# Optimization experiments

Hardware: AMD Instinct MI355X
Metric: run time of the kernel (lower is better)

## Reference

```python
import jax, jax.numpy as jnp
import numpy as np

# Module hyperparameters derived from init_kwargs
G = 100          # grid_size = int(n_samples ** gamma) = int(10000 ** 0.5)
K = 3            # KAN_SPLINE_ORDER
NB = G + K       # num_basis = 103
H = (1.5 - (-0.5)) / G
# grid identical for every input feature (torch expands a 1D grid)
GRID = jnp.arange(-K, G + K + 1, dtype=jnp.float32) * H - 0.5  # (G + 2K + 1,)


def bspline_basis(x):
    """Cox-de Boor recursion. x: (B, F) -> (B, F, NB)."""
    g = GRID
    xe = x[..., None]  # (B, F, 1)
    bases = ((xe >= g[:-1]) & (xe < g[1:])).astype(x.dtype)  # (B, F, G+2K)
    for k in range(1, K + 1):
        left = (xe - g[:-(k + 1)]) / jnp.maximum(g[k:-1] - g[:-(k + 1)], 1e-8)
        right = (g[k + 1:] - xe) / jnp.maximum(g[k + 1:] - g[1:-k], 1e-8)
        bases = left * bases[..., :-1] + right * bases[..., 1:]
    return bases  # (B, F, NB)


def kan_layer(x, bw, sw, wb, ws, residual):
    # base path: SiLU activation then linear
    base_out = jax.nn.silu(x) @ bw.T                      # (B, out)
    # spline path: basis expansion then contraction with spline_weight
    spline_out = jnp.einsum('bin,oin->bo', bspline_basis(x), sw)
    out = wb * base_out + ws * spline_out
    return out + x if residual else out


def setup_inputs() -> dict:
    key = jax.random.key(0)
    ks = jax.random.split(key, 16)
    B, D, W = 2048, 64, 243
    inp = {'x': jax.random.uniform(ks[0], (B, D), dtype=jnp.float32)}
    dims = [(D, W), (W, W), (W, W), (W, W), (W, W), (W, 1)]
    for i, (fi, fo) in enumerate(dims):
        kb, ksw = jax.random.split(jax.random.fold_in(key, i + 1))
        inp[f'bw{i}'] = jax.random.normal(kb, (fo, fi), dtype=jnp.float32) * (1.0 / np.sqrt(fi))
        # torch init: uniform(-0.5/G, 0.5/G)
        inp[f'sw{i}'] = jax.random.uniform(ksw, (fo, fi, NB), dtype=jnp.float32,
                                           minval=-0.5 / G, maxval=0.5 / G)
        inp[f'wb{i}'] = jnp.zeros((1,), dtype=jnp.float32)
        inp[f'ws{i}'] = jnp.ones((1,), dtype=jnp.float32)
    return inp


def reference(x, bw0, sw0, wb0, ws0, bw1, sw1, wb1, ws1, bw2, sw2, wb2, ws2,
              bw3, sw3, wb3, ws3, bw4, sw4, wb4, ws4, bw5, sw5, wb5, ws5):
    layers = [
        (bw0, sw0, wb0, ws0, False),  # 64 -> 243 (in != out: no residual)
        (bw1, sw1, wb1, ws1, True),
        (bw2, sw2, wb2, ws2, True),
        (bw3, sw3, wb3, ws3, True),
        (bw4, sw4, wb4, ws4, True),
        (bw5, sw5, wb5, ws5, False),  # 243 -> 1 (use_residual=False)
    ]
    h = x
    for bw, sw, wb, ws, res in layers:
        h = kan_layer(h, bw, sw, wb, ws, res)
    return h
```

## Files before the change

kernel.cpp:

```cpp
#include <hip/hip_runtime.h>
#include <hip/hip_fp16.h>
#include <math.h>

#define BATCH 2048
#define NBAS 103
#define NPAIR 102
#define OUTR 243
#define OUTP 256

typedef _Float16 half2v __attribute__((ext_vector_type(2)));

__device__ __forceinline__ float dot2(unsigned a, unsigned b, float c) {
#if __has_builtin(__builtin_amdgcn_fdot2)
    return __builtin_amdgcn_fdot2(__builtin_bit_cast(half2v, a),
                                  __builtin_bit_cast(half2v, b), c, false);
#else
    __half2 ha = __builtin_bit_cast(__half2, a), hb = __builtin_bit_cast(__half2, b);
    c = fmaf(__low2float(ha), __low2float(hb), c);
    c = fmaf(__high2float(ha), __high2float(hb), c);
    return c;
#endif
}

__device__ __forceinline__ uint4 make_meta(float x, int i) {
    float u = (x + 0.56f) * 50.0f;
    bool inr = (u >= 0.0f) && (u < 106.0f);
    float fj = floorf(u);
    float t = u - fj;
    int j = (int)fj;
    j = j < -1 ? -1 : (j > 106 ? 106 : j);
    float omt = 1.0f - t;
    float t2 = t * t, t3 = t2 * t;
    float w[4];
    w[0] = omt * omt * omt * (1.0f / 6.0f);
    w[1] = (3.0f * t3 - 6.0f * t2 + 4.0f) * (1.0f / 6.0f);
    w[2] = (-3.0f * t3 + 3.0f * t2 + 3.0f * t + 1.0f) * (1.0f / 6.0f);
    w[3] = t3 * (1.0f / 6.0f);
    int idx = j - 3;
    int idxc = idx < 0 ? 0 : (idx > 99 ? 99 : idx);
    int d = idx - idxc;
    float wc[4];
    #pragma unroll
    for (int m = 0; m < 4; ++m) {
        int s = m - d;
        wc[m] = (inr && s >= 0 && s < 4) ? w[s] : 0.0f;
    }
    __half2 w01 = __floats2half2_rn(wc[0], wc[1]);
    __half2 w23 = __floats2half2_rn(wc[2], wc[3]);
    uint4 m4;
    m4.x = __builtin_bit_cast(unsigned, w01);
    m4.y = __builtin_bit_cast(unsigned, w23);
    m4.z = (unsigned)((i * NPAIR + idxc) << 8);
    m4.w = (unsigned)(i * NBAS + idxc);
    return m4;
}

__device__ __forceinline__ void pairgen_body(
    const float* __restrict__ sw, int IN, unsigned* __restrict__ pairT,
    __half (*tile)[106], int i, int obase)
{
    int nl = threadIdx.x & 63;
    int w = threadIdx.x >> 6;
    #pragma unroll
    for (int k = 0; k < 8; ++k) {
        int r = w * 8 + k;
        int o = obase + r;
        if (o < OUTR) {
            const float* p = sw + ((size_t)o * IN + i) * NBAS;
            tile[r][nl] = __float2half(p[nl]);
            if (nl + 64 < NBAS)
                tile[r][nl + 64] = __float2half(p[nl + 64]);
        }
    }
    __syncthreads();
    unsigned* dst = pairT + (size_t)i * NPAIR * 256 + obase;
    for (int idx = threadIdx.x; idx < NPAIR * 32; idx += 256) {
        int p = idx >> 5, o = idx & 31;
        unsigned v = 0;
        if (obase + o < OUTR) {
            unsigned lo = __half_as_ushort(tile[o][p]);
            unsigned hi = __half_as_ushort(tile[o][p + 1]);
            v = lo | (hi << 16);
        }
        dst[(size_t)p * 256 + o] = v;
    }
}

__global__ __launch_bounds__(256) void pairgen_kernel(
    const float* __restrict__ sw, int IN, unsigned* __restrict__ pairT)
{
    __shared__ __half tile[32][106];
    pairgen_body(sw, IN, pairT, tile, blockIdx.x, blockIdx.y * 32);
}

template <int IN>
__global__ __launch_bounds__(256) void basis_kernel(
    const float* __restrict__ xin, int xstride, uint4* __restrict__ meta,
    float4* __restrict__ zbuf)
{
    int e = blockIdx.x * 256 + threadIdx.x;
    if (zbuf && e < (BATCH * OUTP) / 4) zbuf[e] = make_float4(0.f, 0.f, 0.f, 0.f);
    if (e >= BATCH * IN) return;
    int b = e / IN, i = e - b * IN;
    meta[e] = make_meta(xin[(size_t)b * xstride + i], i);
}

template <bool ADDRES>
__global__ __launch_bounds__(256) void basis_mid_kernel(
    const float* __restrict__ hprev,
    const float* __restrict__ parts,
    uint4* __restrict__ meta, float* __restrict__ hcomb)
{
    int e = blockIdx.x * 256 + threadIdx.x;
    if (e >= BATCH * OUTR) return;
    int b = e / OUTR, i = e - b * OUTR;
    size_t addr = (size_t)b * OUTP + i;
    const size_t PS = (size_t)BATCH * OUTP;
    float h = ADDRES ? hprev[addr] : 0.0f;
    #pragma unroll
    for (int s = 0; s < 8; ++s) h += parts[s * PS + addr];
    hcomb[addr] = h;
    meta[e] = make_meta(h, i);
}

template <bool ADDRES>
__global__ __launch_bounds__(256) void fused_pg_bm_kernel(
    const float* __restrict__ sw, unsigned* __restrict__ pairT,
    const float* __restrict__ hprev, const float* __restrict__ parts,
    uint4* __restrict__ meta, float* __restrict__ hcomb)
{
    if (blockIdx.y == 0) {
        __shared__ __half tile[32][106];
        pairgen_body(sw, OUTR, pairT, tile, blockIdx.x >> 3, (blockIdx.x & 7) * 32);
    } else {
        int e = blockIdx.x * 256 + threadIdx.x;
        if (e >= BATCH * OUTR) return;
        int b = e / OUTR, i = e - b * OUTR;
        size_t addr = (size_t)b * OUTP + i;
        const size_t PS = (size_t)BATCH * OUTP;
        float h = ADDRES ? hprev[addr] : 0.0f;
        #pragma unroll
        for (int s = 0; s < 8; ++s) h += parts[s * PS + addr];
        hcomb[addr] = h;
        meta[e] = make_meta(h, i);
    }
}

__global__ __launch_bounds__(256) void fused0_kernel(
    const float* __restrict__ sw0, unsigned* __restrict__ pairT,
    const float* __restrict__ xin, uint4* __restrict__ meta)
{
    if (blockIdx.y == 0) {
        __shared__ __half tile[32][106];
        pairgen_body(sw0, 64, pairT, tile, blockIdx.x >> 3, (blockIdx.x & 7) * 32);
    } else {
        int e = blockIdx.x * 256 + threadIdx.x;
        int b = e >> 6, i = e & 63;
        meta[e] = make_meta(xin[(size_t)b * 64 + i], i);
    }
}

template <int IN>
__global__ __launch_bounds__(256, 8) void layer_store_kernel(
    const unsigned* __restrict__ pairT, const uint4* __restrict__ meta,
    const float* __restrict__ h_in, int hstride,
    const float* __restrict__ bw,
    const float* __restrict__ wbp, const float* __restrict__ wsp,
    float* __restrict__ part)
{
    const int lane = threadIdx.x & 63;
    const int wave = __builtin_amdgcn_readfirstlane(threadIdx.x >> 6);
    const int b0 = blockIdx.y * 8 + wave * 2;
    const int cx = blockIdx.x;
    const int i0 = (IN * cx) >> 3;
    const int i1 = (IN * (cx + 1)) >> 3;
    const uint4* mp0 = meta + (size_t)b0 * IN;
    const uint4* mp1 = mp0 + IN;
    float a0[4] = {0.f, 0.f, 0.f, 0.f};
    float a1[4] = {0.f, 0.f, 0.f, 0.f};
    #pragma unroll 2
    for (int i = i0; i < i1; ++i) {
        uint4 m0 = mp0[i];
        uint4 m1 = mp1[i];
        const uint4* pA = (const uint4*)(pairT + m0.z) + lane;
        const uint4* pB = (const uint4*)(pairT + m1.z) + lane;
        uint4 ra = pA[0];
        uint4 rb = pA[128];
        uint4 rc = pB[0];
        uint4 rd = pB[128];
        a0[0] = dot2(m0.x, ra.x, a0[0]); a0[1] = dot2(m0.x, ra.y, a0[1]);
        a0[2] = dot2(m0.x, ra.z, a0[2]); a0[3] = dot2(m0.x, ra.w, a0[3]);
        a0[0] = dot2(m0.y, rb.x, a0[0]); a0[1] = dot2(m0.y, rb.y, a0[1]);
        a0[2] = dot2(m0.y, rb.z, a0[2]); a0[3] = dot2(m0.y, rb.w, a0[3]);
        a1[0] = dot2(m1.x, rc.x, a1[0]); a1[1] = dot2(m1.x, rc.y, a1[1]);
        a1[2] = dot2(m1.x, rc.z, a1[2]); a1[3] = dot2(m1.x, rc.w, a1[3]);
        a1[0] = dot2(m1.y, rd.x, a1[0]); a1[1] = dot2(m1.y, rd.y, a1[1]);
        a1[2] = dot2(m1.y, rd.z, a1[2]); a1[3] = dot2(m1.y, rd.w, a1[3]);
    }
    float wsv = wsp[0];
    float wbv = wbp[0];
    float4 v0 = make_float4(wsv * a0[0], wsv * a0[1], wsv * a0[2], wsv * a0[3]);
    float4 v1 = make_float4(wsv * a1[0], wsv * a1[1], wsv * a1[2], wsv * a1[3]);
    if (wbv != 0.0f) {
        float* pv0 = &v0.x; float* pv1 = &v1.x;
        for (int c = 0; c < 4; ++c) {
            int o = lane * 4 + c;
            if (o < OUTR) {
                float bs0 = 0.0f, bs1 = 0.0f;
                for (int i = i0; i < i1; ++i) {
                    float x0 = h_in[(size_t)b0 * hstride + i];
                    float x1 = h_in[(size_t)(b0 + 1) * hstride + i];
                    bs0 = fmaf(x0 / (1.0f + expf(-x0)), bw[o * IN + i], bs0);
                    bs1 = fmaf(x1 / (1.0f + expf(-x1)), bw[o * IN + i], bs1);
                }
                pv0[c] += wbv * bs0;
                pv1[c] += wbv * bs1;
            }
        }
    }
    float* d0 = part + ((size_t)cx * BATCH + b0) * OUTP + lane * 4;
    *(float4*)d0 = v0;
    *(float4*)(d0 + OUTP) = v1;
}

template <int IN, bool RES>
__global__ __launch_bounds__(256, 8) void layer_atomic_kernel(
    const unsigned* __restrict__ pairT, const uint4* __restrict__ meta,
    const float* __restrict__ h_in, int hstride,
    const float* __restrict__ bw,
    const float* __restrict__ wbp, const float* __restrict__ wsp,
    float* __restrict__ out)
{
    const int lane = threadIdx.x & 63;
    const int wave = __builtin_amdgcn_readfirstlane(threadIdx.x >> 6);
    const int b = blockIdx.y * 4 + wave;
    const int cx = blockIdx.x;
    const int i0 = (IN * cx) >> 3;
    const int i1 = (IN * (cx + 1)) >> 3;
    const uint4* mp = meta + (size_t)b * IN;
    float acc[4] = {0.f, 0.f, 0.f, 0.f};
    #pragma unroll 2
    for (int i = i0; i < i1; ++i) {
        uint4 m = mp[i];
        const uint4* pA = (const uint4*)(pairT + m.z) + lane;
        uint4 ra = pA[0];
        uint4 rb = pA[128];
        acc[0] = dot2(m.x, ra.x, acc[0]); acc[1] = dot2(m.x, ra.y, acc[1]);
        acc[2] = dot2(m.x, ra.z, acc[2]); acc[3] = dot2(m.x, ra.w, acc[3]);
        acc[0] = dot2(m.y, rb.x, acc[0]); acc[1] = dot2(m.y, rb.y, acc[1]);
        acc[2] = dot2(m.y, rb.z, acc[2]); acc[3] = dot2(m.y, rb.w, acc[3]);
    }
    float wsv = wsp[0];
    float wbv = wbp[0];
    #pragma unroll
    for (int c = 0; c < 4; ++c) {
        int o = lane * 4 + c;
        float v = wsv * acc[c];
        if (RES && cx == 0) v += h_in[(size_t)b * hstride + o];
        if (wbv != 0.0f && o < OUTR) {
            float bs = 0.0f;
            for (int i = i0; i < i1; ++i) {
                float xx = h_in[(size_t)b * hstride + i];
                bs = fmaf(xx / (1.0f + expf(-xx)), bw[o * IN + i], bs);
            }
            v += wbv * bs;
        }
        unsafeAtomicAdd(&out[(size_t)b * OUTP + o], v);
    }
}

__global__ __launch_bounds__(256) void final_kernel(
    const float* __restrict__ sw5,
    const uint4* __restrict__ meta,
    const float* __restrict__ h, const float* __restrict__ bw5,
    const float* __restrict__ wbp, const float* __restrict__ wsp,
    float* __restrict__ out)
{
    int wave = threadIdx.x >> 6, lane = threadIdx.x & 63;
    int b = blockIdx.x * 4 + wave;
    float s = 0.0f;
    for (int i = lane; i < OUTR; i += 64) {
        uint4 m = meta[(size_t)b * OUTR + i];
        __half2 w01 = __builtin_bit_cast(__half2, m.x);
        __half2 w23 = __builtin_bit_cast(__half2, m.y);
        const float* p = sw5 + m.w;
        s += __low2float(w01) * p[0] + __high2float(w01) * p[1]
           + __low2float(w23) * p[2] + __high2float(w23) * p[3];
    }
    #pragma unroll
    for (int d = 32; d; d >>= 1) s += __shfl_down(s, d, 64);
    if (lane == 0) {
        float v = wsp[0] * s;
        float wbv = wbp[0];
        if (wbv != 0.0f) {
            float bs = 0.0f;
            for (int i = 0; i < OUTR; ++i) {
                float xx = h[(size_t)b * OUTP + i];
                bs = fmaf(xx / (1.0f + expf(-xx)), bw5[i], bs);
            }
            v += wbv * bs;
        }
        out[b] = v;
    }
}

extern "C" void kernel_launch(void* const* d_in, const int* in_sizes, int n_in,
                              void* d_out, int out_size, void* d_ws, size_t ws_size,
                              hipStream_t stream)
{
    const float* x = (const float*)d_in[0];
    const float *bw[6], *sw[6], *wb[6], *ws[6];
    for (int l = 0; l < 6; ++l) {
        bw[l] = (const float*)d_in[1 + 4 * l];
        sw[l] = (const float*)d_in[2 + 4 * l];
        wb[l] = (const float*)d_in[3 + 4 * l];
        ws[l] = (const float*)d_in[4 + 4 * l];
    }
    char* base = (char*)d_ws;
    const size_t PAIR_B = 0;
    const size_t META_B = 25380864;
    unsigned* pairT = (unsigned*)(base + PAIR_B);
    uint4*    meta  = (uint4*)(base + META_B);
    float*    outp  = (float*)d_out;

    const size_t NEED_NEW = 54315008;
    const int NB243 = (BATCH * OUTR + 255) / 256;

    if (ws_size >= NEED_NEW) {
        float* parts = (float*)(base + 33343488);
        float* hcA   = (float*)(base + 50120704);
        float* hcB   = (float*)(base + 52217856);

        fused0_kernel<<<dim3(512, 2), 256, 0, stream>>>(sw[0], pairT, x, meta);
        layer_store_kernel<64><<<dim3(8, BATCH / 8), 256, 0, stream>>>(
            pairT, meta, x, 64, bw[0], wb[0], ws[0], parts);

        float* hin = hcA; float* hout = hcB;
        for (int l = 1; l <= 4; ++l) {
            if (l == 1)
                fused_pg_bm_kernel<false><<<dim3(1944, 2), 256, 0, stream>>>(
                    sw[l], pairT, nullptr, parts, meta, hin);
            else
                fused_pg_bm_kernel<true><<<dim3(1944, 2), 256, 0, stream>>>(
                    sw[l], pairT, hout, parts, meta, hin);
            layer_store_kernel<243><<<dim3(8, BATCH / 8), 256, 0, stream>>>(
                pairT, meta, hin, OUTP, bw[l], wb[l], ws[l], parts);
            float* tmp = hin; hin = hout; hout = tmp;
        }
        basis_mid_kernel<true><<<NB243, 256, 0, stream>>>(hout, parts, meta, hin);
        final_kernel<<<BATCH / 4, 256, 0, stream>>>(sw[5], meta, hin, bw[5], wb[5], ws[5], outp);
    } else {
        if (ws_size < (size_t)37537792) return;
        float* hA = (float*)(base + 33343488);
        float* hB = (float*)(base + 35440640);
        pairgen_kernel<<<dim3(64, 8), 256, 0, stream>>>(sw[0], 64, pairT);
        basis_kernel<64><<<(BATCH * 64) / 256, 256, 0, stream>>>(x, 64, meta, (float4*)hA);
        layer_atomic_kernel<64, false><<<dim3(8, BATCH / 4), 256, 0, stream>>>(
            pairT, meta, x, 64, bw[0], wb[0], ws[0], hA);
        float* hin = hA; float* hout = hB;
        for (int l = 1; l <= 4; ++l) {
            pairgen_kernel<<<dim3(OUTR, 8), 256, 0, stream>>>(sw[l], OUTR, pairT);
            basis_kernel<243><<<NB243, 256, 0, stream>>>(hin, OUTP, meta, (float4*)hout);
            layer_atomic_kernel<243, true><<<dim3(8, BATCH / 4), 256, 0, stream>>>(
                pairT, meta, hin, OUTP, bw[l], wb[l], ws[l], hout);
            float* tmp = hin; hin = hout; hout = tmp;
        }
        basis_kernel<243><<<NB243, 256, 0, stream>>>(hin, OUTP, meta, nullptr);
        final_kernel<<<BATCH / 4, 256, 0, stream>>>(sw[5], meta, hin, bw[5], wb[5], ws[5], outp);
    }
}
```

Baseline: 400.0 us.

## Precompute all layer spline pair tables in one launch and fuse final basis

When the workspace is large enough, a single kernel converts the spline weights of layers 0 to 4 into fp16 pair tables, each in its own buffer, and also builds the layer-0 basis metadata. The per-layer fused pairgen-plus-basis launches become plain basis_mid launches. Separately, the last basis pass and final kernel merge into one kernel that sums the partials, evaluates the basis inline and does the reduction. This removes kernel launches and the serial dependency of each layer's weight conversion on the previous layer, at the cost of about 83 MB more workspace and a large up-front conversion launch. If the harness workspace is smaller, the old path runs with only the final fusion.

```diff
diff --git a/kernel.cpp b/kernel.cpp
--- a/kernel.cpp
+++ b/kernel.cpp
@@ -91,6 +91,36 @@
 {
     __shared__ __half tile[32][106];
     pairgen_body(sw, IN, pairT, tile, blockIdx.x, blockIdx.y * 32);
+}
+
+__global__ __launch_bounds__(256) void pairgen_all_kernel(
+    const float* __restrict__ sw0, const float* __restrict__ sw1,
+    const float* __restrict__ sw2, const float* __restrict__ sw3,
+    const float* __restrict__ sw4,
+    unsigned* __restrict__ pT0, unsigned* __restrict__ pT1,
+    unsigned* __restrict__ pT2, unsigned* __restrict__ pT3,
+    unsigned* __restrict__ pT4,
+    const float* __restrict__ xin, uint4* __restrict__ meta)
+{
+    __shared__ __half tile[32][106];
+    int bx = blockIdx.x;
+    if (bx < 512) {
+        pairgen_body(sw0, 64, pT0, tile, bx >> 3, (bx & 7) * 32);
+    } else if (bx < 8288) {
+        int idx = bx - 512;
+        int l = idx / 1944;
+        int rem = idx - l * 1944;
+        const float* sw; unsigned* pt;
+        if (l == 0)      { sw = sw1; pt = pT1; }
+        else if (l == 1) { sw = sw2; pt = pT2; }
+        else if (l == 2) { sw = sw3; pt = pT3; }
+        else             { sw = sw4; pt = pT4; }
+        pairgen_body(sw, OUTR, pt, tile, rem >> 3, (rem & 7) * 32);
+    } else {
+        int e = (bx - 8288) * 256 + threadIdx.x;
+        int b = e >> 6, i = e & 63;
+        meta[e] = make_meta(xin[(size_t)b * 64 + i], i);
+    }
 }
 
 template <int IN>
@@ -269,6 +299,39 @@
     }
 }
 
+__global__ __launch_bounds__(256) void final_fused_kernel(
+    const float* __restrict__ sw5,
+    const float* __restrict__ hprev,
+    const float* __restrict__ parts,
+    const float* __restrict__ bw5,
+    const float* __restrict__ wbp, const float* __restrict__ wsp,
+    float* __restrict__ out)
+{
+    int wave = threadIdx.x >> 6, lane = threadIdx.x & 63;
+    int b = blockIdx.x * 4 + wave;
+    const size_t PS = (size_t)BATCH * OUTP;
+    float s = 0.0f, bs = 0.0f;
+    for (int i = lane; i < OUTR; i += 64) {
+        size_t addr = (size_t)b * OUTP + i;
+        float h = hprev[addr];
+        #pragma unroll
+        for (int ss = 0; ss < 8; ++ss) h += parts[ss * PS + addr];
+        uint4 m = make_meta(h, i);
+        __half2 w01 = __builtin_bit_cast(__half2, m.x);
+        __half2 w23 = __builtin_bit_cast(__half2, m.y);
+        const float* p = sw5 + m.w;
+        s += __low2float(w01) * p[0] + __high2float(w01) * p[1]
+           + __low2float(w23) * p[2] + __high2float(w23) * p[3];
+        bs = fmaf(h / (1.0f + expf(-h)), bw5[i], bs);
+    }
+    #pragma unroll
+    for (int d = 32; d; d >>= 1) {
+        s += __shfl_down(s, d, 64);
+        bs += __shfl_down(bs, d, 64);
+    }
+    if (lane == 0) out[b] = wsp[0] * s + wbp[0] * bs;
+}
+
 __global__ __launch_bounds__(256) void final_kernel(
     const float* __restrict__ sw5,
     const uint4* __restrict__ meta,
@@ -317,52 +380,81 @@
         ws[l] = (const float*)d_in[4 + 4 * l];
     }
     char* base = (char*)d_ws;
-    const size_t PAIR_B = 0;
-    const size_t META_B = 25380864;
-    unsigned* pairT = (unsigned*)(base + PAIR_B);
-    uint4*    meta  = (uint4*)(base + META_B);
-    float*    outp  = (float*)d_out;
-
-    const size_t NEED_NEW = 54315008;
+    unsigned* pairT1 = (unsigned*)(base + 0);
+    uint4*    meta   = (uint4*)(base + 25380864);
+    float*    outp   = (float*)d_out;
     const int NB243 = (BATCH * OUTR + 255) / 256;
 
-    if (ws_size >= NEED_NEW) {
+    const size_t NEED_ALL = 137142272;
+    const size_t NEED_MID = 54315008;
+    const size_t NEED_ATM = 37537792;
+
+    if (ws_size >= NEED_ALL) {
+        float*    parts  = (float*)(base + 33343488);
+        float*    hcA    = (float*)(base + 50120704);
+        float*    hcB    = (float*)(base + 52217856);
+        unsigned* pairT0 = (unsigned*)(base + 54315008);
+        unsigned* pairT2 = (unsigned*)(base + 60999680);
+        unsigned* pairT3 = (unsigned*)(base + 86380544);
+        unsigned* pairT4 = (unsigned*)(base + 111761408);
+        unsigned* pT[5] = {pairT0, pairT1, pairT2, pairT3, pairT4};
+
+        pairgen_all_kernel<<<8800, 256, 0, stream>>>(
+            sw[0], sw[1], sw[2], sw[3], sw[4],
+            pairT0, pairT1, pairT2, pairT3, pairT4, x, meta);
+
+        layer_store_kernel<64><<<dim3(8, BATCH / 8), 256, 0, stream>>>(
+            pairT0, meta, x, 64, bw[0], wb[0], ws[0], parts);
+
+        float* hin = hcA; float* hout = hcB;
+        for (int l = 1; l <= 4; ++l) {
+            if (l == 1)
+                basis_mid_kernel<false><<<NB243, 256, 0, stream>>>(nullptr, parts, meta, hin);
+            else
+                basis_mid_kernel<true><<<NB243, 256, 0, stream>>>(hout, parts, meta, hin);
+            layer_store_kernel<243><<<dim3(8, BATCH / 8), 256, 0, stream>>>(
+                pT[l], meta, hin, OUTP, bw[l], wb[l], ws[l], parts);
+            float* tmp = hin; hin = hout; hout = tmp;
+        }
+        final_fused_kernel<<<BATCH / 4, 256, 0, stream>>>(
+            sw[5], hout, parts, bw[5], wb[5], ws[5], outp);
+    } else if (ws_size >= NEED_MID) {
         float* parts = (float*)(base + 33343488);
         float* hcA   = (float*)(base + 50120704);
         float* hcB   = (float*)(base + 52217856);
 
-        fused0_kernel<<<dim3(512, 2), 256, 0, stream>>>(sw[0], pairT, x, meta);
+        fused0_kernel<<<dim3(512, 2), 256, 0, stream>>>(sw[0], pairT1, x, meta);
         layer_store_kernel<64><<<dim3(8, BATCH / 8), 256, 0, stream>>>(
-            pairT, meta, x, 64, bw[0], wb[0], ws[0], parts);
+            pairT1, meta, x, 64, bw[0], wb[0], ws[0], parts);
 
         float* hin = hcA; float* hout = hcB;
         for (int l = 1; l <= 4; ++l) {
             if (l == 1)
                 fused_pg_bm_kernel<false><<<dim3(1944, 2), 256, 0, stream>>>(
-                    sw[l], pairT, nullptr, parts, meta, hin);
+                    sw[l], pairT1, nullptr, parts, meta, hin);
             else
                 fused_pg_bm_kernel<true><<<dim3(1944, 2), 256, 0, stream>>>(
-                    sw[l], pairT, hout, parts, meta, hin);
+                    sw[l], pairT1, hout, parts, meta, hin);
             layer_store_kernel<243><<<dim3(8, BATCH / 8), 256, 0, stream>>>(
-                pairT, meta, hin, OUTP, bw[l], wb[l], ws[l], parts);
+                pairT1, meta, hin, OUTP, bw[l], wb[l], ws[l], parts);
             float* tmp = hin; hin = hout; hout = tmp;
         }
-        basis_mid_kernel<true><<<NB243, 256, 0, stream>>>(hout, parts, meta, hin);
-        final_kernel<<<BATCH / 4, 256, 0, stream>>>(sw[5], meta, hin, bw[5], wb[5], ws[5], outp);
+        final_fused_kernel<<<BATCH / 4, 256, 0, stream>>>(
+            sw[5], hout, parts, bw[5], wb[5], ws[5], outp);
     } else {
-        if (ws_size < (size_t)37537792) return;
+        if (ws_size < NEED_ATM) return;
         float* hA = (float*)(base + 33343488);
         float* hB = (float*)(base + 35440640);
-        pairgen_kernel<<<dim3(64, 8), 256, 0, stream>>>(sw[0], 64, pairT);
+        pairgen_kernel<<<dim3(64, 8), 256, 0, stream>>>(sw[0], 64, pairT1);
         basis_kernel<64><<<(BATCH * 64) / 256, 256, 0, stream>>>(x, 64, meta, (float4*)hA);
         layer_atomic_kernel<64, false><<<dim3(8, BATCH / 4), 256, 0, stream>>>(
-            pairT, meta, x, 64, bw[0], wb[0], ws[0], hA);
+            pairT1, meta, x, 64, bw[0], wb[0], ws[0], hA);
         float* hin = hA; float* hout = hB;
         for (int l = 1; l <= 4; ++l) {
-            pairgen_kernel<<<dim3(OUTR, 8), 256, 0, stream>>>(sw[l], OUTR, pairT);
+            pairgen_kernel<<<dim3(OUTR, 8), 256, 0, stream>>>(sw[l], OUTR, pairT1);
             basis_kernel<243><<<NB243, 256, 0, stream>>>(hin, OUTP, meta, (float4*)hout);
             layer_atomic_kernel<243, true><<<dim3(8, BATCH / 4), 256, 0, stream>>>(
-                pairT, meta, hin, OUTP, bw[l], wb[l], ws[l], hout);
+                pairT1, meta, hin, OUTP, bw[l], wb[l], ws[l], hout);
             float* tmp = hin; hin = hout; hout = tmp;
         }
         basis_kernel<243><<<NB243, 256, 0, stream>>>(hin, OUTP, meta, nullptr);
```

Result: no change. 403.3 us (+0.8%).
